# Kernel optimization log

Hardware: AMD Instinct MI355X
Metric: run time of the kernel (lower is better)

## Reference

```python
import jax, jax.numpy as jnp
import numpy as np

NT, NV, ND, NM, NP = 50000, 1000, 20000, 5000, 8000
E = 100000
D, H, C = 256, 4, 64          # gnn_hidden_dim, heads, per-head channels
TS_FEAT, EMB, L = 64, 128, 2
NEG_SLOPE = 0.2

SIZES = {'ts': NT, 'vital': NV, 'diag': ND, 'med': NM, 'proc': NP}
EDGE_TYPES = [('ts', 'vital'), ('vital', 'ts'), ('ts', 'diag'), ('diag', 'ts'),
              ('ts', 'med'), ('med', 'ts'), ('ts', 'proc'), ('proc', 'ts')]
T = len(EDGE_TYPES)


def setup_inputs():
    key = jax.random.key(0)
    ks = jax.random.split(key, 32)
    def nrm(k, shape, s=0.05):
        return jax.random.normal(k, shape, dtype=jnp.float32) * s
    inp = {}
    inp['ts_x'] = nrm(ks[0], (NT, TS_FEAT), 1.0)
    inp['emb_vital'] = nrm(ks[1], (NV, EMB), 1.0)
    inp['emb_diag'] = nrm(ks[2], (ND, EMB), 1.0)
    inp['emb_med'] = nrm(ks[3], (NM, EMB), 1.0)
    inp['emb_proc'] = nrm(ks[4], (NP, EMB), 1.0)
    inp['Wp_ts'] = nrm(ks[5], (TS_FEAT, D)); inp['bp_ts'] = jnp.zeros((D,), jnp.float32)
    inp['Wp_c'] = nrm(ks[6], (4, EMB, D)); inp['bp_c'] = jnp.zeros((4, D), jnp.float32)
    inp['Wsrc'] = nrm(ks[7], (L, T, D, H * C))
    inp['Wdst'] = nrm(ks[8], (L, T, D, H * C))
    inp['asrc'] = nrm(ks[9], (L, T, H, C))
    inp['adst'] = nrm(ks[10], (L, T, H, C))
    inp['bconv'] = jnp.zeros((L, T, H * C), jnp.float32)
    inp['Wc1'] = nrm(ks[11], (D, D // 2)); inp['bc1'] = jnp.zeros((D // 2,), jnp.float32)
    inp['Wc2'] = nrm(ks[12], (D // 2, 1)); inp['bc2'] = jnp.zeros((1,), jnp.float32)
    names = ['ei_tv', 'ei_vt', 'ei_td', 'ei_dt', 'ei_tm', 'ei_mt', 'ei_tp', 'ei_pt']
    for i, ((s, d), nm) in enumerate(zip(EDGE_TYPES, names)):
        k1, k2 = jax.random.split(ks[13 + i])
        src = jax.random.randint(k1, (E,), 0, SIZES[s], dtype=jnp.int32)
        dst = jax.random.randint(k2, (E,), 0, SIZES[d], dtype=jnp.int32)
        inp[nm] = jnp.stack([src, dst])
    return inp


def gat_conv(xs, xd, Ws, Wd, a_s, a_d, b, ei, nd):
    """Bipartite PyG GATConv: add_self_loops=False, concat heads, eval (no dropout)."""
    hs = (xs @ Ws).reshape(-1, H, C)            # [Ns,H,C]
    hd = (xd @ Wd).reshape(-1, H, C)            # [Nd,H,C]
    es = jnp.sum(hs * a_s, axis=-1)             # [Ns,H]
    ed = jnp.sum(hd * a_d, axis=-1)             # [Nd,H]
    src, dst = ei[0], ei[1]
    e = jax.nn.leaky_relu(es[src] + ed[dst], NEG_SLOPE)   # [E,H]
    m = jax.ops.segment_max(e, dst, num_segments=nd)      # segment softmax over dst
    ex = jnp.exp(e - m[dst])
    den = jax.ops.segment_sum(ex, dst, num_segments=nd)
    alpha = ex / (den[dst] + 1e-16)
    msg = (alpha[:, :, None] * hs[src]).reshape(-1, H * C)  # [E,H*C]
    return jax.ops.segment_sum(msg, dst, num_segments=nd) + b


def _forward(ts_x, emb_vital, emb_diag, emb_med, emb_proc, Wp_ts, bp_ts, Wp_c, bp_c,
             Wsrc, Wdst, asrc, adst, bconv, Wc1, bc1, Wc2, bc2, edges):
    x = {'ts': ts_x @ Wp_ts + bp_ts,
         'vital': emb_vital @ Wp_c[0] + bp_c[0],
         'diag': emb_diag @ Wp_c[1] + bp_c[1],
         'med': emb_med @ Wp_c[2] + bp_c[2],
         'proc': emb_proc @ Wp_c[3] + bp_c[3]}
    for l in range(L):
        new = {k: jnp.zeros((SIZES[k], D), jnp.float32) for k in x}  # HeteroConv aggr='sum'
        for t, ((s, d), ei) in enumerate(zip(EDGE_TYPES, edges)):
            new[d] = new[d] + gat_conv(x[s], x[d], Wsrc[l, t], Wdst[l, t],
                                       asrc[l, t], adst[l, t], bconv[l, t], ei, SIZES[d])
        x = {k: jax.nn.relu(v) for k, v in new.items()}
    g = jnp.mean(x['ts'], axis=0)               # graph embedding
    h = jax.nn.relu(g @ Wc1 + bc1)
    logits = h @ Wc2 + bc2
    return jnp.squeeze(logits, -1)              # output_classes == 1 -> scalar


def reference(ts_x, emb_vital, emb_diag, emb_med, emb_proc, Wp_ts, bp_ts, Wp_c, bp_c,
              Wsrc, Wdst, asrc, adst, bconv, Wc1, bc1, Wc2, bc2,
              ei_tv, ei_vt, ei_td, ei_dt, ei_tm, ei_mt, ei_tp, ei_pt):
    edges = (ei_tv, ei_vt, ei_td, ei_dt, ei_tm, ei_mt, ei_tp, ei_pt)
    return _forward(ts_x, emb_vital, emb_diag, emb_med, emb_proc, Wp_ts, bp_ts, Wp_c, bp_c,
                    Wsrc, Wdst, asrc, adst, bconv, Wc1, bc1, Wc2, bc2, edges)
```

## Files before the change

kernel.cpp:

```cpp
#include <hip/hip_runtime.h>

#define E_N 100000
#define NTOT 84000
#define NDST 234000

typedef __attribute__((ext_vector_type(8))) short bfrag8;
typedef __attribute__((ext_vector_type(4))) float accf4;

__device__ __forceinline__ void atomAddF(float* p, float v) {
    unsafeAtomicAdd(p, v);
}

__device__ __forceinline__ float lrelu(float v) { return v >= 0.f ? v : 0.2f * v; }

__device__ __forceinline__ unsigned short f2bf(float f) {
    unsigned u = __float_as_uint(f);
    return (unsigned short)((u + 0x7FFFu + ((u >> 16) & 1u)) >> 16);
}
__device__ __forceinline__ float bf2f(unsigned short h) {
    return __uint_as_float(((unsigned)h) << 16);
}

__constant__ int c_tbase[8] = {0, 1000, 51000, 71000, 121000, 126000, 176000, 184000};

struct EI8 { const int* p[8]; };

struct BTJob { const float* W; unsigned short* hi; unsigned short* lo; int K; int kshift; };
struct BTBatch { BTJob j[17]; };

__global__ __launch_bounds__(256) void makeBT(BTBatch b)
{
    BTJob jb = b.j[blockIdx.z];
    int idx = blockIdx.x * 256 + threadIdx.x;
    if (idx >= (jb.K << 8)) return;
    int n = idx >> jb.kshift;
    int k = idx & (jb.K - 1);
    float w = jb.W[(size_t)k * 256 + n];
    unsigned short h = f2bf(w);
    jb.hi[idx] = h;
    jb.lo[idx] = f2bf(w - bf2f(h));
}

struct MJob { const float* A; const unsigned short* BThi; const unsigned short* BTlo;
              float* C; const float* bias; int M; int K; int relu; };
struct MBatch { MJob j[8]; };

__global__ __launch_bounds__(256, 2) void gemm_mfma(MBatch batch)
{
    const MJob jb = batch.j[blockIdx.z];
    const int bm = blockIdx.x * 128;
    if (bm >= jb.M) return;
    const int bn = blockIdx.y * 128;
    const int M = jb.M, K = jb.K;

    __shared__ unsigned short Ah[128 * 40];
    __shared__ unsigned short Al[128 * 40];
    __shared__ unsigned short B1[128 * 40];
    __shared__ unsigned short B2[128 * 40];

    const int tid  = threadIdx.x;
    const int wv   = tid >> 6;
    const int lane = tid & 63;
    const int qr = wv >> 1, qc = wv & 1;
    const int lm = lane & 15;
    const int lq = lane >> 4;

    accf4 acc[4][4] = {};

    for (int k0 = 0; k0 < K; k0 += 32) {
#pragma unroll
        for (int it = 0; it < 4; ++it) {
            int slot = it * 256 + tid;
            int m  = slot >> 3;
            int kq = (slot & 7) << 2;
            float4 v = make_float4(0.f, 0.f, 0.f, 0.f);
            if (bm + m < M) v = *(const float4*)(jb.A + (size_t)(bm + m) * K + k0 + kq);
            int o = m * 40 + kq;
            unsigned short h0 = f2bf(v.x), h1 = f2bf(v.y), h2 = f2bf(v.z), h3 = f2bf(v.w);
            Ah[o + 0] = h0; Ah[o + 1] = h1; Ah[o + 2] = h2; Ah[o + 3] = h3;
            Al[o + 0] = f2bf(v.x - bf2f(h0));
            Al[o + 1] = f2bf(v.y - bf2f(h1));
            Al[o + 2] = f2bf(v.z - bf2f(h2));
            Al[o + 3] = f2bf(v.w - bf2f(h3));
        }
#pragma unroll
        for (int it = 0; it < 2; ++it) {
            int slot = it * 256 + tid;
            int n  = slot >> 2;
            int kq = (slot & 3) << 3;
            size_t go = (size_t)(bn + n) * K + k0 + kq;
            *(uint4*)&B1[n * 40 + kq] = *(const uint4*)(jb.BThi + go);
            *(uint4*)&B2[n * 40 + kq] = *(const uint4*)(jb.BTlo + go);
        }
        __syncthreads();

        bfrag8 ah[4], al[4], b1[4], b2[4];
#pragma unroll
        for (int t = 0; t < 4; ++t) {
            int am  = qr * 64 + t * 16 + lm;
            int bnn = qc * 64 + t * 16 + lm;
            ah[t] = *(const bfrag8*)&Ah[am * 40 + lq * 8];
            al[t] = *(const bfrag8*)&Al[am * 40 + lq * 8];
            b1[t] = *(const bfrag8*)&B1[bnn * 40 + lq * 8];
            b2[t] = *(const bfrag8*)&B2[bnn * 40 + lq * 8];
        }
#pragma unroll
        for (int mt = 0; mt < 4; ++mt)
#pragma unroll
            for (int nt = 0; nt < 4; ++nt) {
                acc[mt][nt] = __builtin_amdgcn_mfma_f32_16x16x32_bf16(ah[mt], b1[nt], acc[mt][nt], 0, 0, 0);
                acc[mt][nt] = __builtin_amdgcn_mfma_f32_16x16x32_bf16(al[mt], b1[nt], acc[mt][nt], 0, 0, 0);
                acc[mt][nt] = __builtin_amdgcn_mfma_f32_16x16x32_bf16(ah[mt], b2[nt], acc[mt][nt], 0, 0, 0);
            }
        __syncthreads();
    }

#pragma unroll
    for (int nt = 0; nt < 4; ++nt) {
        int col = bn + qc * 64 + nt * 16 + lm;
        float bv = jb.bias ? jb.bias[col] : 0.f;
#pragma unroll
        for (int mt = 0; mt < 4; ++mt) {
            int row0 = bm + qr * 64 + mt * 16 + lq * 4;
#pragma unroll
            for (int r = 0; r < 4; ++r) {
                int row = row0 + r;
                if (row < M) {
                    float o = acc[mt][nt][r] + bv;
                    if (jb.relu) o = fmaxf(o, 0.f);
                    jb.C[(size_t)row * 256 + col] = o;
                }
            }
        }
    }
}

__global__ __launch_bounds__(256) void fill_weff(const float* __restrict__ Wsrc,
                                                 const float* __restrict__ Wdst,
                                                 const float* __restrict__ asrc,
                                                 const float* __restrict__ adst,
                                                 float* __restrict__ weff)
{
    int idx = blockIdx.x * 256 + threadIdx.x;
    if (idx >= 81920) return;
    int col = idx & 31;
    int k   = (idx >> 5) & 255;
    int lnt = idx >> 13;
    int nt  = lnt % 5;
    int l   = lnt / 5;
    bool is_src; int t, h;
    if (nt == 0) {
        if (col < 16) { is_src = true;  t = (col >> 2) * 2;            h = col & 3; }
        else          { is_src = false; t = ((col - 16) >> 2) * 2 + 1; h = col & 3; }
    } else {
        if (col < 4)      { is_src = true;  t = 2 * nt - 1; h = col; }
        else if (col < 8) { is_src = false; t = 2 * nt - 2; h = col - 4; }
        else { weff[idx] = 0.f; return; }
    }
    const float* W = (is_src ? Wsrc : Wdst) + ((size_t)((l * 8 + t) * 256 + k)) * 256 + h * 64;
    const float* a = (is_src ? asrc : adst) + ((size_t)((l * 8 + t) * 4 + h)) * 64;
    float val = 0.f;
    for (int c = 0; c < 64; c++) val += W[c] * a[c];
    weff[idx] = val;
}

template<int NO>
__device__ __forceinline__ void attnproj_body(const float* __restrict__ xrow,
                                              const float* __restrict__ W,
                                              float* __restrict__ out)
{
    float acc[NO];
#pragma unroll
    for (int j = 0; j < NO; j++) acc[j] = 0.f;
    for (int k = 0; k < 256; k += 4) {
        const float4 xv = *(const float4*)(xrow + k);
#pragma unroll
        for (int j = 0; j < NO; j++) {
            acc[j] += xv.x * W[(k + 0) * 32 + j] + xv.y * W[(k + 1) * 32 + j]
                    + xv.z * W[(k + 2) * 32 + j] + xv.w * W[(k + 3) * 32 + j];
        }
    }
#pragma unroll
    for (int j = 0; j < NO; j++) out[j] = acc[j];
}

__global__ __launch_bounds__(256) void attnproj(const float* __restrict__ x,
                                                const float* __restrict__ weff_l,
                                                float* __restrict__ attnT,
                                                float* __restrict__ attnC)
{
    int n = blockIdx.x * 256 + threadIdx.x;
    if (n >= NTOT) return;
    if (n < 50000) {
        attnproj_body<32>(x + (size_t)n * 256, weff_l, attnT + (size_t)n * 32);
    } else {
        int nt = (n < 51000) ? 1 : (n < 71000) ? 2 : (n < 76000) ? 3 : 4;
        attnproj_body<8>(x + (size_t)n * 256, weff_l + nt * 8192, attnC + (size_t)(n - 50000) * 8);
    }
}

__global__ __launch_bounds__(256) void count_k(EI8 ei, int* __restrict__ cnt)
{
    int g = blockIdx.x * 256 + threadIdx.x;
    if (g >= 8 * E_N) return;
    int t = g / E_N;
    int i = g - t * E_N;
    int d = ei.p[t][E_N + i];
    atomicAdd(&cnt[c_tbase[t] + d], 1);
}

__global__ __launch_bounds__(256) void scanA(const int* __restrict__ cnt,
                                             int* __restrict__ rowptr,
                                             int* __restrict__ bsum)
{
    __shared__ int sd[256];
    int b = blockIdx.x, t = threadIdx.x;
    int base = b * 1024 + t * 4;
    int v0 = 0, v1 = 0, v2 = 0, v3 = 0;
    if (base + 0 < NDST) v0 = cnt[base + 0];
    if (base + 1 < NDST) v1 = cnt[base + 1];
    if (base + 2 < NDST) v2 = cnt[base + 2];
    if (base + 3 < NDST) v3 = cnt[base + 3];
    int s = v0 + v1 + v2 + v3;
    sd[t] = s;
    __syncthreads();
    for (int off = 1; off < 256; off <<= 1) {
        int x = 0;
        if (t >= off) x = sd[t - off];
        __syncthreads();
        if (t >= off) sd[t] += x;
        __syncthreads();
    }
    int run = sd[t] - s;
    if (t == 255) bsum[b] = sd[255];
    if (base + 0 < NDST) rowptr[base + 0] = run;          run += v0;
    if (base + 1 < NDST) rowptr[base + 1] = run;          run += v1;
    if (base + 2 < NDST) rowptr[base + 2] = run;          run += v2;
    if (base + 3 < NDST) rowptr[base + 3] = run;
}

__global__ __launch_bounds__(256) void scanB(int* __restrict__ bsum, int nb)
{
    __shared__ int sd[256];
    int t = threadIdx.x;
    int v = (t < nb) ? bsum[t] : 0;
    sd[t] = v;
    __syncthreads();
    for (int off = 1; off < 256; off <<= 1) {
        int x = 0;
        if (t >= off) x = sd[t - off];
        __syncthreads();
        if (t >= off) sd[t] += x;
        __syncthreads();
    }
    if (t < nb) bsum[t] = sd[t] - v;
}

__global__ __launch_bounds__(256) void scanC(int* __restrict__ rowptr,
                                             const int* __restrict__ bsum,
                                             int* __restrict__ cursor)
{
    int b = blockIdx.x, t = threadIdx.x;
    int off = bsum[b];
    int base = b * 1024 + t * 4;
#pragma unroll
    for (int j = 0; j < 4; j++) {
        int i = base + j;
        if (i < NDST) {
            int r = rowptr[i] + off;
            rowptr[i] = r;
            cursor[i] = r;
        }
    }
    if (b == 0 && t == 0) rowptr[NDST] = 8 * E_N;
}

__global__ __launch_bounds__(256) void place_k(EI8 ei, int* __restrict__ cursor,
                                               int* __restrict__ ssrc)
{
    int g = blockIdx.x * 256 + threadIdx.x;
    if (g >= 8 * E_N) return;
    int t = g / E_N;
    int i = g - t * E_N;
    int d = ei.p[t][E_N + i];
    int s = ei.p[t][i];
    int pos = atomicAdd(&cursor[c_tbase[t] + d], 1);
    ssrc[pos] = s;
}

__global__ __launch_bounds__(256) void aggx_k(const float* __restrict__ attnT,
                                              const float* __restrict__ attnC,
                                              const float* __restrict__ xts,
                                              const int* __restrict__ rowptr,
                                              const int* __restrict__ ssrc,
                                              float* __restrict__ aggx)
{
    int w = blockIdx.x * 4 + (threadIdx.x >> 6);
    int lane = threadIdx.x & 63;
    int h = lane >> 4;
    int ch = (h << 6) | ((lane & 15) << 2);
    int q, dloc;
    if (w < 1000)       { q = 0; dloc = w; }
    else if (w < 21000) { q = 1; dloc = w - 1000; }
    else if (w < 26000) { q = 2; dloc = w - 21000; }
    else                { q = 3; dloc = w - 26000; }
    const int csr4[4]  = {0, 51000, 121000, 176000};
    const int soff4[4] = {0, 4, 8, 12};
    int r0 = rowptr[csr4[q] + dloc], r1 = rowptr[csr4[q] + dloc + 1];
    float ed = attnC[(size_t)w * 8 + 4 + h];
    float den = 0.f, sx = 0.f, sy = 0.f, sz = 0.f, sw = 0.f;
    for (int e = r0; e < r1; e++) {
        int s = ssrc[e];
        float es = attnT[(size_t)s * 32 + soff4[q] + h];
        float ex = __expf(lrelu(es + ed));
        den += ex;
        const float4 xv = *(const float4*)(xts + (size_t)s * 256 + ch);
        sx += ex * xv.x; sy += ex * xv.y; sz += ex * xv.z; sw += ex * xv.w;
    }
    float inv = 1.f / (den + 1e-16f);
    float4 o; o.x = sx * inv; o.y = sy * inv; o.z = sz * inv; o.w = sw * inv;
    *(float4*)(aggx + (size_t)w * 256 + ch) = o;
}

__global__ __launch_bounds__(256) void agg_ts(const float* __restrict__ attnT,
                                              const float* __restrict__ attnC,
                                              const float* __restrict__ hsc,
                                              const int* __restrict__ rowptr,
                                              const int* __restrict__ ssrc,
                                              const float* __restrict__ bconv_l,
                                              float* __restrict__ xout)
{
    int d = blockIdx.x * 4 + (threadIdx.x >> 6);
    int lane = threadIdx.x & 63;
    int h = lane >> 4;
    int ch = (h << 6) | ((lane & 15) << 2);
    const int co4[4]   = {0, 1000, 21000, 26000};
    const int tb4[4]   = {1000, 71000, 126000, 184000};
    const int doff4[4] = {16, 20, 24, 28};
    const int bo4[4]   = {256, 768, 1280, 1792};
    float ax = 0.f, ay = 0.f, az = 0.f, aw = 0.f;
#pragma unroll
    for (int q = 0; q < 4; q++) {
        const float* b = bconv_l + bo4[q] + ch;
        ax += b[0]; ay += b[1]; az += b[2]; aw += b[3];
    }
#pragma unroll
    for (int q = 0; q < 4; q++) {
        int r0 = rowptr[tb4[q] + d], r1 = rowptr[tb4[q] + d + 1];
        float ed = attnT[(size_t)d * 32 + doff4[q] + h];
        float den = 0.f, sx = 0.f, sy = 0.f, sz = 0.f, sw = 0.f;
        for (int e = r0; e < r1; e++) {
            int s = ssrc[e];
            float es = attnC[(size_t)(co4[q] + s) * 8 + h];
            float ex = __expf(lrelu(es + ed));
            den += ex;
            const float4 hv = *(const float4*)(hsc + (size_t)(co4[q] + s) * 256 + ch);
            sx += ex * hv.x; sy += ex * hv.y; sz += ex * hv.z; sw += ex * hv.w;
        }
        float inv = 1.f / (den + 1e-16f);
        ax += sx * inv; ay += sy * inv; az += sz * inv; aw += sw * inv;
    }
    float4 o;
    o.x = fmaxf(ax, 0.f); o.y = fmaxf(ay, 0.f);
    o.z = fmaxf(az, 0.f); o.w = fmaxf(aw, 0.f);
    *(float4*)(xout + (size_t)d * 256 + ch) = o;
}

__global__ __launch_bounds__(256) void colsum_ts(const float* __restrict__ x,
                                                 float* __restrict__ gsum)
{
    int c = threadIdx.x;
    float s = 0.f;
    for (int r = blockIdx.x; r < 50000; r += gridDim.x) s += x[(size_t)r * 256 + c];
    atomAddF(gsum + c, s);
}

__global__ __launch_bounds__(128) void head_k(const float* __restrict__ gsum,
                                              const float* __restrict__ Wc1,
                                              const float* __restrict__ bc1,
                                              const float* __restrict__ Wc2,
                                              const float* __restrict__ bc2,
                                              float* __restrict__ out)
{
    __shared__ float g[256];
    __shared__ float red[128];
    int t = threadIdx.x;
    g[t] = gsum[t] * (1.f / 50000.f);
    g[t + 128] = gsum[t + 128] * (1.f / 50000.f);
    __syncthreads();
    float acc = bc1[t];
    for (int k = 0; k < 256; k++) acc += g[k] * Wc1[k * 128 + t];
    red[t] = fmaxf(acc, 0.f) * Wc2[t];
    __syncthreads();
    for (int sft = 64; sft > 0; sft >>= 1) {
        if (t < sft) red[t] += red[t + sft];
        __syncthreads();
    }
    if (t == 0) out[0] = red[0] + bc2[0];
}

extern "C" void kernel_launch(void* const* d_in, const int* in_sizes, int n_in,
                              void* d_out, int out_size, void* d_ws, size_t ws_size,
                              hipStream_t stream)
{
    const float* ts_x   = (const float*)d_in[0];
    const float* emb[4] = {(const float*)d_in[1], (const float*)d_in[2],
                           (const float*)d_in[3], (const float*)d_in[4]};
    const float* Wp_ts  = (const float*)d_in[5];
    const float* bp_ts  = (const float*)d_in[6];
    const float* Wp_c   = (const float*)d_in[7];
    const float* bp_c   = (const float*)d_in[8];
    const float* Wsrc   = (const float*)d_in[9];
    const float* Wdst   = (const float*)d_in[10];
    const float* asrc   = (const float*)d_in[11];
    const float* adst   = (const float*)d_in[12];
    const float* bconv  = (const float*)d_in[13];
    const float* Wc1    = (const float*)d_in[14];
    const float* bc1    = (const float*)d_in[15];
    const float* Wc2    = (const float*)d_in[16];
    const float* bc2    = (const float*)d_in[17];
    EI8 ei;
    for (int t = 0; t < 8; t++) ei.p[t] = (const int*)d_in[18 + t];

    float* x0    = (float*)d_ws;
    float* x1    = x0    + 21504000;
    float* hsc   = x1    + 21504000;
    float* attnT = hsc   + 8704000;
    float* attnC = attnT + 1600000;
    float* weff  = attnC + 272000;
    float* gsum  = weff  + 81920;
    int* rowptr  = (int*)(gsum + 256);
    int* bsum    = rowptr + 234004;
    int* ssrc    = bsum + 256;
    unsigned short* btp = (unsigned short*)(ssrc + 800000);
    int* cursor  = (int*)hsc;
    float* aggx  = x1;

    unsigned short* bt_ts_h = btp;
    unsigned short* bt_ts_l = bt_ts_h + 16384;
    unsigned short* bt_c_h[4], *bt_c_l[4];
    {
        unsigned short* p = bt_ts_l + 16384;
        for (int q = 0; q < 4; q++) { bt_c_h[q] = p; p += 32768; bt_c_l[q] = p; p += 32768; }
    }
    unsigned short* bt_w = bt_ts_l + 16384 + 8 * 32768;
    auto wpan_h = [&](int l, int t) { return bt_w + (size_t)((l == 0 ? t : 8 + t / 2) * 2) * 65536; };
    auto wpan_l = [&](int l, int t) { return wpan_h(l, t) + 65536; };

    hipMemsetAsync(cursor, 0, NDST * sizeof(int), stream);
    count_k<<<3125, 256, 0, stream>>>(ei, cursor);
    scanA<<<229, 256, 0, stream>>>(cursor, rowptr, bsum);
    scanB<<<1, 256, 0, stream>>>(bsum, 229);
    scanC<<<229, 256, 0, stream>>>(rowptr, bsum, cursor);
    place_k<<<3125, 256, 0, stream>>>(ei, cursor, ssrc);

    {
        BTBatch b = {};
        int zi = 0;
        b.j[zi++] = {Wp_ts, bt_ts_h, bt_ts_l, 64, 6};
        for (int q = 0; q < 4; q++)
            b.j[zi++] = {Wp_c + q * 32768, bt_c_h[q], bt_c_l[q], 128, 7};
        for (int t = 0; t < 8; t++)
            b.j[zi++] = {Wsrc + (size_t)(0 * 8 + t) * 65536, wpan_h(0, t), wpan_l(0, t), 256, 8};
        for (int t = 1; t < 8; t += 2)
            b.j[zi++] = {Wsrc + (size_t)(1 * 8 + t) * 65536, wpan_h(1, t), wpan_l(1, t), 256, 8};
        makeBT<<<dim3(256, 1, 17), 256, 0, stream>>>(b);
    }

    fill_weff<<<320, 256, 0, stream>>>(Wsrc, Wdst, asrc, adst, weff);

    static const int Nd4[4]    = {1000, 20000, 5000, 8000};
    static const int co4[4]    = {0, 1000, 21000, 26000};
    static const int dbase4[4] = {50000, 51000, 71000, 76000};
    static const int tsrc[4]   = {1, 3, 5, 7};
    static const int tdst[4]   = {0, 2, 4, 6};

    {
        MBatch b = {};
        b.j[0] = {ts_x, bt_ts_h, bt_ts_l, x0, bp_ts, 50000, 64, 0};
        for (int q = 0; q < 4; q++)
            b.j[1 + q] = {emb[q], bt_c_h[q], bt_c_l[q], x0 + (size_t)dbase4[q] * 256,
                          bp_c + q * 256, Nd4[q], 128, 0};
        gemm_mfma<<<dim3(391, 2, 5), 256, 0, stream>>>(b);
    }

    attnproj<<<329, 256, 0, stream>>>(x0, weff, attnT, attnC);
    aggx_k<<<8500, 256, 0, stream>>>(attnT, attnC, x0, rowptr, ssrc, aggx);
    {
        MBatch b = {};
        for (int q = 0; q < 4; q++)
            b.j[q] = {x0 + (size_t)dbase4[q] * 256, wpan_h(0, tsrc[q]), wpan_l(0, tsrc[q]),
                      hsc + (size_t)co4[q] * 256, nullptr, Nd4[q], 256, 0};
        for (int q = 0; q < 4; q++)
            b.j[4 + q] = {aggx + (size_t)co4[q] * 256, wpan_h(0, tdst[q]), wpan_l(0, tdst[q]),
                          x1 + (size_t)dbase4[q] * 256, bconv + tdst[q] * 256, Nd4[q], 256, 1};
        gemm_mfma<<<dim3(157, 2, 8), 256, 0, stream>>>(b);
    }
    agg_ts<<<12500, 256, 0, stream>>>(attnT, attnC, hsc, rowptr, ssrc, bconv, x1);

    attnproj<<<329, 256, 0, stream>>>(x1, weff + 40960, attnT, attnC);
    {
        MBatch b = {};
        for (int q = 0; q < 4; q++)
            b.j[q] = {x1 + (size_t)dbase4[q] * 256, wpan_h(1, tsrc[q]), wpan_l(1, tsrc[q]),
                      hsc + (size_t)co4[q] * 256, nullptr, Nd4[q], 256, 0};
        gemm_mfma<<<dim3(157, 2, 4), 256, 0, stream>>>(b);
    }
    agg_ts<<<12500, 256, 0, stream>>>(attnT, attnC, hsc, rowptr, ssrc, bconv + 2048, x0);

    hipMemsetAsync(gsum, 0, 256 * sizeof(float), stream);
    colsum_ts<<<256, 256, 0, stream>>>(x0, gsum);
    head_k<<<1, 128, 0, stream>>>(gsum, Wc1, bc1, Wc2, bc2, (float*)d_out);
}
```

Measured before the change: 796.1 us.

## Store gathered node features in bf16 and unroll edge aggregation loops

```diff
diff --git a/kernel.cpp b/kernel.cpp
--- a/kernel.cpp
+++ b/kernel.cpp
@@ -42,7 +42,7 @@
 }
 
 struct MJob { const float* A; const unsigned short* BThi; const unsigned short* BTlo;
-              float* C; const float* bias; int M; int K; int relu; };
+              float* C; unsigned short* Cbf; const float* bias; int M; int K; int relu; };
 struct MBatch { MJob j[8]; };
 
 __global__ __launch_bounds__(256, 2) void gemm_mfma(MBatch batch)
@@ -128,7 +128,8 @@
                 if (row < M) {
                     float o = acc[mt][nt][r] + bv;
                     if (jb.relu) o = fmaxf(o, 0.f);
-                    jb.C[(size_t)row * 256 + col] = o;
+                    if (jb.C)   jb.C[(size_t)row * 256 + col] = o;
+                    if (jb.Cbf) jb.Cbf[(size_t)row * 256 + col] = f2bf(o);
                 }
             }
         }
@@ -290,7 +291,7 @@
 
 __global__ __launch_bounds__(256) void aggx_k(const float* __restrict__ attnT,
                                               const float* __restrict__ attnC,
-                                              const float* __restrict__ xts,
+                                              const unsigned short* __restrict__ xtsbf,
                                               const int* __restrict__ rowptr,
                                               const int* __restrict__ ssrc,
                                               float* __restrict__ aggx)
@@ -306,16 +307,39 @@
     else                { q = 3; dloc = w - 26000; }
     const int csr4[4]  = {0, 51000, 121000, 176000};
     const int soff4[4] = {0, 4, 8, 12};
+    int soff = soff4[q];
     int r0 = rowptr[csr4[q] + dloc], r1 = rowptr[csr4[q] + dloc + 1];
     float ed = attnC[(size_t)w * 8 + 4 + h];
     float den = 0.f, sx = 0.f, sy = 0.f, sz = 0.f, sw = 0.f;
-    for (int e = r0; e < r1; e++) {
+    int e = r0;
+    for (; e + 4 <= r1; e += 4) {
+        int sA = ssrc[e], sB = ssrc[e + 1], sC = ssrc[e + 2], sD = ssrc[e + 3];
+        float eA = attnT[(size_t)sA * 32 + soff + h];
+        float eB = attnT[(size_t)sB * 32 + soff + h];
+        float eC = attnT[(size_t)sC * 32 + soff + h];
+        float eD = attnT[(size_t)sD * 32 + soff + h];
+        ushort4 rA = *(const ushort4*)(xtsbf + (size_t)sA * 256 + ch);
+        ushort4 rB = *(const ushort4*)(xtsbf + (size_t)sB * 256 + ch);
+        ushort4 rC = *(const ushort4*)(xtsbf + (size_t)sC * 256 + ch);
+        ushort4 rD = *(const ushort4*)(xtsbf + (size_t)sD * 256 + ch);
+        float xA = __expf(lrelu(eA + ed));
+        float xB = __expf(lrelu(eB + ed));
+        float xC = __expf(lrelu(eC + ed));
+        float xD = __expf(lrelu(eD + ed));
+        den += (xA + xB) + (xC + xD);
+        sx += xA * bf2f(rA.x) + xB * bf2f(rB.x) + xC * bf2f(rC.x) + xD * bf2f(rD.x);
+        sy += xA * bf2f(rA.y) + xB * bf2f(rB.y) + xC * bf2f(rC.y) + xD * bf2f(rD.y);
+        sz += xA * bf2f(rA.z) + xB * bf2f(rB.z) + xC * bf2f(rC.z) + xD * bf2f(rD.z);
+        sw += xA * bf2f(rA.w) + xB * bf2f(rB.w) + xC * bf2f(rC.w) + xD * bf2f(rD.w);
+    }
+    for (; e < r1; e++) {
         int s = ssrc[e];
-        float es = attnT[(size_t)s * 32 + soff4[q] + h];
+        float es = attnT[(size_t)s * 32 + soff + h];
         float ex = __expf(lrelu(es + ed));
         den += ex;
-        const float4 xv = *(const float4*)(xts + (size_t)s * 256 + ch);
-        sx += ex * xv.x; sy += ex * xv.y; sz += ex * xv.z; sw += ex * xv.w;
+        ushort4 rv = *(const ushort4*)(xtsbf + (size_t)s * 256 + ch);
+        sx += ex * bf2f(rv.x); sy += ex * bf2f(rv.y);
+        sz += ex * bf2f(rv.z); sw += ex * bf2f(rv.w);
     }
     float inv = 1.f / (den + 1e-16f);
     float4 o; o.x = sx * inv; o.y = sy * inv; o.z = sz * inv; o.w = sw * inv;
@@ -324,7 +348,7 @@
 
 __global__ __launch_bounds__(256) void agg_ts(const float* __restrict__ attnT,
                                               const float* __restrict__ attnC,
-                                              const float* __restrict__ hsc,
+                                              const unsigned short* __restrict__ hscbf,
                                               const int* __restrict__ rowptr,
                                               const int* __restrict__ ssrc,
                                               const float* __restrict__ bconv_l,
@@ -338,27 +362,40 @@
     const int tb4[4]   = {1000, 71000, 126000, 184000};
     const int doff4[4] = {16, 20, 24, 28};
     const int bo4[4]   = {256, 768, 1280, 1792};
+
+    int r0q[4], nq[4]; float edq[4];
+    int mx = 0;
+#pragma unroll
+    for (int q = 0; q < 4; q++) {
+        int a = rowptr[tb4[q] + d], b = rowptr[tb4[q] + d + 1];
+        r0q[q] = a; nq[q] = b - a;
+        mx = max(mx, b - a);
+        edq[q] = attnT[(size_t)d * 32 + doff4[q] + h];
+    }
+    float den[4] = {0.f, 0.f, 0.f, 0.f};
+    float sx[4] = {0.f, 0.f, 0.f, 0.f}, sy[4] = {0.f, 0.f, 0.f, 0.f};
+    float sz[4] = {0.f, 0.f, 0.f, 0.f}, sw[4] = {0.f, 0.f, 0.f, 0.f};
+    for (int i = 0; i < mx; i++) {
+#pragma unroll
+        for (int q = 0; q < 4; q++) {
+            if (i < nq[q]) {
+                int s = ssrc[r0q[q] + i];
+                float es = attnC[(size_t)(co4[q] + s) * 8 + h];
+                float ex = __expf(lrelu(es + edq[q]));
+                den[q] += ex;
+                ushort4 hv = *(const ushort4*)(hscbf + (size_t)(co4[q] + s) * 256 + ch);
+                sx[q] += ex * bf2f(hv.x); sy[q] += ex * bf2f(hv.y);
+                sz[q] += ex * bf2f(hv.z); sw[q] += ex * bf2f(hv.w);
+            }
+        }
+    }
     float ax = 0.f, ay = 0.f, az = 0.f, aw = 0.f;
 #pragma unroll
     for (int q = 0; q < 4; q++) {
         const float* b = bconv_l + bo4[q] + ch;
-        ax += b[0]; ay += b[1]; az += b[2]; aw += b[3];
-    }
-#pragma unroll
-    for (int q = 0; q < 4; q++) {
-        int r0 = rowptr[tb4[q] + d], r1 = rowptr[tb4[q] + d + 1];
-        float ed = attnT[(size_t)d * 32 + doff4[q] + h];
-        float den = 0.f, sx = 0.f, sy = 0.f, sz = 0.f, sw = 0.f;
-        for (int e = r0; e < r1; e++) {
-            int s = ssrc[e];
-            float es = attnC[(size_t)(co4[q] + s) * 8 + h];
-            float ex = __expf(lrelu(es + ed));
-            den += ex;
-            const float4 hv = *(const float4*)(hsc + (size_t)(co4[q] + s) * 256 + ch);
-            sx += ex * hv.x; sy += ex * hv.y; sz += ex * hv.z; sw += ex * hv.w;
-        }
-        float inv = 1.f / (den + 1e-16f);
-        ax += sx * inv; ay += sy * inv; az += sz * inv; aw += sw * inv;
+        float inv = 1.f / (den[q] + 1e-16f);
+        ax += b[0] + sx[q] * inv; ay += b[1] + sy[q] * inv;
+        az += b[2] + sz[q] * inv; aw += b[3] + sw[q] * inv;
     }
     float4 o;
     o.x = fmaxf(ax, 0.f); o.y = fmaxf(ay, 0.f);
@@ -424,16 +461,17 @@
 
     float* x0    = (float*)d_ws;
     float* x1    = x0    + 21504000;
-    float* hsc   = x1    + 21504000;
-    float* attnT = hsc   + 8704000;
+    float* attnT = x1    + 21504000;
     float* attnC = attnT + 1600000;
     float* weff  = attnC + 272000;
     float* gsum  = weff  + 81920;
     int* rowptr  = (int*)(gsum + 256);
     int* bsum    = rowptr + 234004;
     int* ssrc    = bsum + 256;
-    unsigned short* btp = (unsigned short*)(ssrc + 800000);
-    int* cursor  = (int*)hsc;
+    unsigned short* xtsbf = (unsigned short*)(ssrc + 800000);
+    unsigned short* hscbf = xtsbf + 12800000;
+    unsigned short* btp   = hscbf + 8704000;
+    int* cursor  = (int*)hscbf;
     float* aggx  = x1;
 
     unsigned short* bt_ts_h = btp;
@@ -477,36 +515,36 @@
 
     {
         MBatch b = {};
-        b.j[0] = {ts_x, bt_ts_h, bt_ts_l, x0, bp_ts, 50000, 64, 0};
+        b.j[0] = {ts_x, bt_ts_h, bt_ts_l, x0, xtsbf, bp_ts, 50000, 64, 0};
         for (int q = 0; q < 4; q++)
             b.j[1 + q] = {emb[q], bt_c_h[q], bt_c_l[q], x0 + (size_t)dbase4[q] * 256,
-                          bp_c + q * 256, Nd4[q], 128, 0};
+                          nullptr, bp_c + q * 256, Nd4[q], 128, 0};
         gemm_mfma<<<dim3(391, 2, 5), 256, 0, stream>>>(b);
     }
 
     attnproj<<<329, 256, 0, stream>>>(x0, weff, attnT, attnC);
-    aggx_k<<<8500, 256, 0, stream>>>(attnT, attnC, x0, rowptr, ssrc, aggx);
+    aggx_k<<<8500, 256, 0, stream>>>(attnT, attnC, xtsbf, rowptr, ssrc, aggx);
     {
         MBatch b = {};
         for (int q = 0; q < 4; q++)
             b.j[q] = {x0 + (size_t)dbase4[q] * 256, wpan_h(0, tsrc[q]), wpan_l(0, tsrc[q]),
-                      hsc + (size_t)co4[q] * 256, nullptr, Nd4[q], 256, 0};
+                      nullptr, hscbf + (size_t)co4[q] * 256, nullptr, Nd4[q], 256, 0};
         for (int q = 0; q < 4; q++)
             b.j[4 + q] = {aggx + (size_t)co4[q] * 256, wpan_h(0, tdst[q]), wpan_l(0, tdst[q]),
-                          x1 + (size_t)dbase4[q] * 256, bconv + tdst[q] * 256, Nd4[q], 256, 1};
+                          x1 + (size_t)dbase4[q] * 256, nullptr, bconv + tdst[q] * 256, Nd4[q], 256, 1};
         gemm_mfma<<<dim3(157, 2, 8), 256, 0, stream>>>(b);
     }
-    agg_ts<<<12500, 256, 0, stream>>>(attnT, attnC, hsc, rowptr, ssrc, bconv, x1);
+    agg_ts<<<12500, 256, 0, stream>>>(attnT, attnC, hscbf, rowptr, ssrc, bconv, x1);
 
     attnproj<<<329, 256, 0, stream>>>(x1, weff + 40960, attnT, attnC);
     {
         MBatch b = {};
         for (int q = 0; q < 4; q++)
             b.j[q] = {x1 + (size_t)dbase4[q] * 256, wpan_h(1, tsrc[q]), wpan_l(1, tsrc[q]),
-                      hsc + (size_t)co4[q] * 256, nullptr, Nd4[q], 256, 0};
+                      nullptr, hscbf + (size_t)co4[q] * 256, nullptr, Nd4[q], 256, 0};
         gemm_mfma<<<dim3(157, 2, 4), 256, 0, stream>>>(b);
     }
-    agg_ts<<<12500, 256, 0, stream>>>(attnT, attnC, hsc, rowptr, ssrc, bconv + 2048, x0);
+    agg_ts<<<12500, 256, 0, stream>>>(attnT, attnC, hscbf, rowptr, ssrc, bconv + 2048, x0);
 
     hipMemsetAsync(gsum, 0, 256 * sizeof(float), stream);
     colsum_ts<<<256, 256, 0, stream>>>(x0, gsum);
```

Measured after the change: 756.7 us. -4.9%, faster.
